# Optimization experiments

Hardware: AMD Instinct MI355X
Metric: run time of the kernel (lower is better)

The kernel has to match this reference:

```python
import jax, jax.numpy as jnp
import numpy as np

N_NODES = 50000
N_EDGES = 1600000
D = 64
F = 8
K = 16384


def setup_inputs() -> dict:
    key = jax.random.key(0)
    k1, k2, k3, k4, k5 = jax.random.split(key, 5)
    raw_data = jax.random.randint(k1, (N_NODES,), 0, F, dtype=jnp.int64) if jax.config.jax_enable_x64 else jax.random.randint(k1, (N_NODES,), 0, F, dtype=jnp.int32)
    edge_src = jax.random.randint(k2, (N_EDGES,), 0, N_NODES, dtype=jnp.int32)
    edge_dst = jax.random.randint(k3, (N_EDGES,), 0, N_NODES, dtype=jnp.int32)
    edge_vals = jax.random.normal(k4, (N_EDGES, D), dtype=jnp.float32)
    core_idxs = jax.random.randint(k5, (K,), 0, N_NODES, dtype=jnp.int32)
    return {
        "raw_data": raw_data,
        "edge_src": edge_src,
        "edge_dst": edge_dst,
        "edge_vals": edge_vals,
        "core_idxs": core_idxs,
        "feature_type_count": F,
    }


def reference(raw_data, edge_src, edge_dst, edge_vals, core_idxs, feature_type_count):
    # For each feature type f and origin node i:
    #   out[i, f, :] = max over edges (i -> j) of (edge_vals * [raw_data[j] == f])
    # Origins with no edges at all are zero (torch zero-init of max_res).
    n_nodes = raw_data.shape[0]
    dst_type = raw_data[edge_dst]  # [E] feature type of each edge's neighbor
    outs = []
    for f in range(feature_type_count):  # small fixed loop over feature types
        mask = (dst_type == f).astype(edge_vals.dtype)          # [E]
        masked = edge_vals * mask[:, None]                       # [E, D]
        seg = jax.ops.segment_max(masked, edge_src, num_segments=n_nodes)  # [N, D]
        seg = jnp.where(jnp.isneginf(seg), jnp.zeros((), seg.dtype), seg)  # empty origins -> 0
        outs.append(seg[core_idxs])                              # [K, D]
    return jnp.stack(outs, axis=1)  # [K, F, D]
```

## Files before the change

### kernel.cpp

```cpp
#include <hip/hip_runtime.h>

#define NNODES 50000
#define FT 8
#define DD 64
#define KK 16384
#define CAPF 64
#define OVFCAP 32768
#define NBW 1568


__global__ void init_kernel(int* __restrict__ cnt, int* __restrict__ bits,
                            int* __restrict__ head, int* __restrict__ gtot) {
    int i = blockIdx.x * 256 + threadIdx.x;
    if (i < NNODES * FT) cnt[i] = 0;
    if (i < NBW) bits[i] = 0;
    if (i < NNODES) head[i] = -1;
    if (i < 4) gtot[i] = 0;
}

__global__ void mark_kernel(const int* __restrict__ core, int* __restrict__ bits,
                            int* __restrict__ head, int* __restrict__ nxt,
                            int* __restrict__ slot_node, int* __restrict__ gtot) {
    int k = blockIdx.x * 256 + threadIdx.x;
    if (k >= KK) return;
    int node = core[k];
    nxt[k] = atomicExch(&head[node], k);
    unsigned bit = 1u << (node & 31);
    unsigned old = atomicOr((unsigned*)&bits[node >> 5], bit);
    if (!(old & bit)) {
        int s = atomicAdd(&gtot[1], 1);
        slot_node[s] = node;
    }
}

__global__ void scatter_kernel(const int4* __restrict__ esrc4, const int4* __restrict__ edst4,
                               const int* __restrict__ rawd, const int* __restrict__ bits,
                               int* __restrict__ cnt, int* __restrict__ sorted,
                               int* __restrict__ gtot, int* __restrict__ ovf_key,
                               int* __restrict__ ovf_e, int nE) {
    int t = blockIdx.x * 256 + threadIdx.x;
    int e = t * 4;
    if (e >= nE) return;
    if (e + 3 < nE) {
        int4 s = esrc4[t];
        int4 d = edst4[t];
        int sv[4] = {s.x, s.y, s.z, s.w};
        int dv[4] = {d.x, d.y, d.z, d.w};
#pragma unroll
        for (int j = 0; j < 4; ++j) {
            int sn = sv[j];
            if (!((((unsigned)bits[sn >> 5]) >> (sn & 31)) & 1u)) continue;
            int cell = sn * FT + rawd[dv[j]];
            int p = atomicAdd(&cnt[cell], 1);
            if (p < CAPF) {
                sorted[(size_t)cell * CAPF + p] = e + j;
            } else {
                int q = atomicAdd(&gtot[0], 1);
                if (q < OVFCAP) { ovf_key[q] = cell; ovf_e[q] = e + j; }
            }
        }
    } else {
        const int* esrc = (const int*)esrc4;
        const int* edst = (const int*)edst4;
        for (; e < nE; ++e) {
            int sn = esrc[e];
            if (!((((unsigned)bits[sn >> 5]) >> (sn & 31)) & 1u)) continue;
            int cell = sn * FT + rawd[edst[e]];
            int p = atomicAdd(&cnt[cell], 1);
            if (p < CAPF) {
                sorted[(size_t)cell * CAPF + p] = e;
            } else {
                int q = atomicAdd(&gtot[0], 1);
                if (q < OVFCAP) { ovf_key[q] = cell; ovf_e[q] = e; }
            }
        }
    }
}

__global__ void compute_kernel(const int* __restrict__ slot_node, const int* __restrict__ cnt,
                               const int* __restrict__ sorted, const int* __restrict__ head,
                               const int* __restrict__ nxt, const float* __restrict__ evals,
                               const int* __restrict__ gtot, const int* __restrict__ ovf_key,
                               const int* __restrict__ ovf_e, float* __restrict__ out) {
    int wave = (blockIdx.x * blockDim.x + threadIdx.x) >> 6;
    int lane = threadIdx.x & 63;
    if (wave >= gtot[1]) return;
    int node = __builtin_amdgcn_readfirstlane(slot_node[wave]);

    int cf[FT];
    int deg = 0;
    bool anyovf = false;
#pragma unroll
    for (int f = 0; f < FT; ++f) {
        cf[f] = __builtin_amdgcn_readfirstlane(cnt[node * FT + f]);
        deg += cf[f];
        anyovf |= (cf[f] > CAPF);
    }

    float rmax[FT];
#pragma unroll
    for (int f = 0; f < FT; ++f) {
        int n = cf[f] < CAPF ? cf[f] : CAPF;
        const int* bkt = sorted + ((size_t)node * FT + f) * CAPF;
        float m0 = -INFINITY, m1 = -INFINITY, m2 = -INFINITY, m3 = -INFINITY;
        int i = 0;
        for (; i + 3 < n; i += 4) {
            int4 q = *(const int4*)(bkt + i);
            int e0 = __builtin_amdgcn_readfirstlane(q.x);
            int e1 = __builtin_amdgcn_readfirstlane(q.y);
            int e2 = __builtin_amdgcn_readfirstlane(q.z);
            int e3 = __builtin_amdgcn_readfirstlane(q.w);
            m0 = fmaxf(m0, evals[(size_t)e0 * DD + lane]);
            m1 = fmaxf(m1, evals[(size_t)e1 * DD + lane]);
            m2 = fmaxf(m2, evals[(size_t)e2 * DD + lane]);
            m3 = fmaxf(m3, evals[(size_t)e3 * DD + lane]);
        }
        for (; i < n; ++i) {
            int e0 = __builtin_amdgcn_readfirstlane(bkt[i]);
            m0 = fmaxf(m0, evals[(size_t)e0 * DD + lane]);
        }
        rmax[f] = fmaxf(fmaxf(m0, m1), fmaxf(m2, m3));
    }

    if (anyovf) {
        int no = gtot[0]; if (no > OVFCAP) no = OVFCAP;
        for (int q = 0; q < no; ++q) {
            int key = ovf_key[q];
            if ((key >> 3) != node) continue;
            int f = key & 7;
            float v = evals[(size_t)ovf_e[q] * DD + lane];
#pragma unroll
            for (int t = 0; t < FT; ++t)
                if (t == f) rmax[t] = fmaxf(rmax[t], v);
        }
    }

    float res[FT];
#pragma unroll
    for (int f = 0; f < FT; ++f) {
        int matched = cf[f];
        float val;
        if (matched == 0)        val = 0.0f;
        else if (matched < deg)  val = fmaxf(rmax[f], 0.0f);
        else                     val = rmax[f];
        res[f] = val;
    }

    for (int k = head[node]; k >= 0; k = nxt[k]) {
        float* op = out + (size_t)k * (FT * DD) + lane;
#pragma unroll
        for (int f = 0; f < FT; ++f) op[f * DD] = res[f];
    }
}

extern "C" void kernel_launch(void* const* d_in, const int* in_sizes, int n_in,
                              void* d_out, int out_size, void* d_ws, size_t ws_size,
                              hipStream_t stream) {
    const int*   rawd  = (const int*)d_in[0];
    const int*   esrc  = (const int*)d_in[1];
    const int*   edst  = (const int*)d_in[2];
    const float* evals = (const float*)d_in[3];
    const int*   core  = (const int*)d_in[4];
    int nE = in_sizes[1];

    int* wsi       = (int*)d_ws;
    int* cnt       = wsi;
    int* bits      = wsi + 400000;
    int* head      = wsi + 401568;
    int* nxt       = wsi + 451568;
    int* slot_node = wsi + 467952;
    int* gtot      = wsi + 484336;
    int* ovf_key   = wsi + 484340;
    int* ovf_e     = wsi + 517108;
    int* sorted    = wsi + 549888;

    init_kernel<<<(NNODES * FT + 255) / 256, 256, 0, stream>>>(cnt, bits, head, gtot);
    mark_kernel<<<(KK + 255) / 256, 256, 0, stream>>>(core, bits, head, nxt, slot_node, gtot);

    int nE4 = (nE + 3) / 4;
    scatter_kernel<<<(nE4 + 255) / 256, 256, 0, stream>>>(
        (const int4*)esrc, (const int4*)edst, rawd, bits, cnt, sorted,
        gtot, ovf_key, ovf_e, nE);

    long long cthreads = (long long)KK * 64;
    compute_kernel<<<(int)((cthreads + 255) / 256), 256, 0, stream>>>(
        slot_node, cnt, sorted, head, nxt, evals, gtot, ovf_key, ovf_e, (float*)d_out);
}
```

Measured before the change: 75.88 us.

## Shrink bucket capacity and preload first eight edge ids per feature up front

Reduces per-cell bucket capacity from 64 to 16, shrinking the sorted workspace and its write footprint. The compute kernel now loads the 8 counts with two int4 loads and prefetches the first 8 edge indices of every feature bucket before any gathers. It then issues the evals gathers unrolled and predicated, which exposes more independent loads. Average edges per cell here are about 4, so overflow stays rare, but nodes with high-degree cells fall into the slow serial overflow scan.

```diff
diff --git a/kernel.cpp b/kernel.cpp
--- a/kernel.cpp
+++ b/kernel.cpp
@@ -4,7 +4,7 @@
 #define FT 8
 #define DD 64
 #define KK 16384
-#define CAPF 64
+#define CAPF 16
 #define OVFCAP 32768
 #define NBW 1568
 
@@ -77,6 +77,8 @@
     }
 }
 
+#define RL(x) __builtin_amdgcn_readfirstlane(x)
+
 __global__ void compute_kernel(const int* __restrict__ slot_node, const int* __restrict__ cnt,
                                const int* __restrict__ sorted, const int* __restrict__ head,
                                const int* __restrict__ nxt, const float* __restrict__ evals,
@@ -85,39 +87,39 @@
     int wave = (blockIdx.x * blockDim.x + threadIdx.x) >> 6;
     int lane = threadIdx.x & 63;
     if (wave >= gtot[1]) return;
-    int node = __builtin_amdgcn_readfirstlane(slot_node[wave]);
+    int node = RL(slot_node[wave]);
 
-    int cf[FT];
+    const int4* c4 = (const int4*)(cnt + node * FT);
+    int4 cA = c4[0], cB = c4[1];
+    int cf[FT] = { RL(cA.x), RL(cA.y), RL(cA.z), RL(cA.w),
+                   RL(cB.x), RL(cB.y), RL(cB.z), RL(cB.w) };
     int deg = 0;
     bool anyovf = false;
 #pragma unroll
-    for (int f = 0; f < FT; ++f) {
-        cf[f] = __builtin_amdgcn_readfirstlane(cnt[node * FT + f]);
-        deg += cf[f];
-        anyovf |= (cf[f] > CAPF);
-    }
+    for (int f = 0; f < FT; ++f) { deg += cf[f]; anyovf |= (cf[f] > CAPF); }
+
+    const int4* bkt4 = (const int4*)(sorted + (size_t)node * FT * CAPF);
+    int4 id0[FT], id1[FT];
+#pragma unroll
+    for (int f = 0; f < FT; ++f) { id0[f] = bkt4[f * 4]; id1[f] = bkt4[f * 4 + 1]; }
 
     float rmax[FT];
 #pragma unroll
     for (int f = 0; f < FT; ++f) {
         int n = cf[f] < CAPF ? cf[f] : CAPF;
-        const int* bkt = sorted + ((size_t)node * FT + f) * CAPF;
         float m0 = -INFINITY, m1 = -INFINITY, m2 = -INFINITY, m3 = -INFINITY;
-        int i = 0;
-        for (; i + 3 < n; i += 4) {
-            int4 q = *(const int4*)(bkt + i);
-            int e0 = __builtin_amdgcn_readfirstlane(q.x);
-            int e1 = __builtin_amdgcn_readfirstlane(q.y);
-            int e2 = __builtin_amdgcn_readfirstlane(q.z);
-            int e3 = __builtin_amdgcn_readfirstlane(q.w);
-            m0 = fmaxf(m0, evals[(size_t)e0 * DD + lane]);
-            m1 = fmaxf(m1, evals[(size_t)e1 * DD + lane]);
-            m2 = fmaxf(m2, evals[(size_t)e2 * DD + lane]);
-            m3 = fmaxf(m3, evals[(size_t)e3 * DD + lane]);
-        }
-        for (; i < n; ++i) {
-            int e0 = __builtin_amdgcn_readfirstlane(bkt[i]);
-            m0 = fmaxf(m0, evals[(size_t)e0 * DD + lane]);
+        if (n > 0) m0 = evals[(size_t)RL(id0[f].x) * DD + lane];
+        if (n > 1) m1 = evals[(size_t)RL(id0[f].y) * DD + lane];
+        if (n > 2) m2 = evals[(size_t)RL(id0[f].z) * DD + lane];
+        if (n > 3) m3 = evals[(size_t)RL(id0[f].w) * DD + lane];
+        if (n > 4) m0 = fmaxf(m0, evals[(size_t)RL(id1[f].x) * DD + lane]);
+        if (n > 5) m1 = fmaxf(m1, evals[(size_t)RL(id1[f].y) * DD + lane]);
+        if (n > 6) m2 = fmaxf(m2, evals[(size_t)RL(id1[f].z) * DD + lane]);
+        if (n > 7) m3 = fmaxf(m3, evals[(size_t)RL(id1[f].w) * DD + lane]);
+        if (n > 8) {
+            const int* bkt = sorted + ((size_t)node * FT + f) * CAPF;
+            for (int i = 8; i < n; ++i)
+                m0 = fmaxf(m0, evals[(size_t)RL(bkt[i]) * DD + lane]);
         }
         rmax[f] = fmaxf(fmaxf(m0, m1), fmaxf(m2, m3));
     }
@@ -127,11 +129,11 @@
         for (int q = 0; q < no; ++q) {
             int key = ovf_key[q];
             if ((key >> 3) != node) continue;
-            int f = key & 7;
+            int fo = key & 7;
             float v = evals[(size_t)ovf_e[q] * DD + lane];
 #pragma unroll
             for (int t = 0; t < FT; ++t)
-                if (t == f) rmax[t] = fmaxf(rmax[t], v);
+                if (t == fo) rmax[t] = fmaxf(rmax[t], v);
         }
     }
 
```

After: 71.71 us. 1.06x faster.
